# Kernel optimization log

Hardware: AMD Instinct MI355X
Metric: run time of the kernel (lower is better)

Reference implementation:

```python
import jax, jax.numpy as jnp
import numpy as np

B, S, HID = 4, 2048, 1024
NH, HD = 16, 64  # op_heads, head_size (hidden_size // total_heads)
EPS = 1e-6


def setup_inputs() -> dict:
    key = jax.random.key(0)
    k1, k2, k3, k4 = jax.random.split(key, 4)
    return {
        "hidden_states": jax.random.normal(k1, (B, S, HID), dtype=jnp.float32),
        "assoc_hc_attn": jax.random.uniform(k2, (B, S, S), dtype=jnp.float32),
        "broad_hc_attn": jax.random.uniform(k3, (B, S, S), dtype=jnp.float32),
        "Wv": jax.random.normal(k4, (HID, NH * HD), dtype=jnp.float32) * 0.02,
        "bv": jnp.zeros((NH * HD,), dtype=jnp.float32),
    }


def reference(hidden_states, assoc_hc_attn, broad_hc_attn, Wv, bv):
    # v_proj + split heads -> [B, NH, S, HD]
    value = hidden_states @ Wv + bv
    sp_value = value.reshape(B, S, NH, HD).transpose(0, 2, 1, 3)

    # broad_heads == 0, so attn_heads == assoc_hc_attn broadcast over all op_heads.
    attn = assoc_hc_attn.astype(jnp.float32)  # [B, S, S]
    causal = jnp.tril(jnp.ones((S, S), dtype=bool))
    attn = jnp.where(causal, attn, 0.0)
    # sum-normalize along keys (no softmax)
    attn = attn / (EPS + attn.sum(axis=-1, keepdims=True))

    # shared attn across heads: contract once -> [B, NH, S, HD]
    out = jnp.einsum('bqk,bhkd->bhqd', attn, sp_value)
    # merge heads -> [B, S, NH*HD]
    return out.transpose(0, 2, 1, 3).reshape(B, S, NH * HD)
```

## Files before the change

### kernel.cpp

```cpp
#include <hip/hip_runtime.h>

#define B_    4
#define S_    2048
#define HID_  1024
#define NO_   1024
#define EPS_  1e-6f
#define M1_   (B_ * S_)

typedef __attribute__((ext_vector_type(8))) short  short8;
typedef __attribute__((ext_vector_type(4))) float  f32x4;
typedef unsigned short ushort_t;

__device__ __forceinline__ unsigned short f2bf(float f) {
  union { float f; unsigned int u; } v; v.f = f;
  unsigned int r = v.u + 0x7FFFu + ((v.u >> 16) & 1u);
  return (unsigned short)(r >> 16);
}
__device__ __forceinline__ unsigned pack2(float a, float b) {
  return (unsigned)f2bf(a) | ((unsigned)f2bf(b) << 16);
}

typedef __attribute__((address_space(1))) const void GASV;
typedef __attribute__((address_space(3))) void LASV;
__device__ __forceinline__ void gld16(const void* g, void* l) {
  __builtin_amdgcn_global_load_lds((GASV*)g, (LASV*)l, 16, 0, 0);
}

__global__ __launch_bounds__(256) void k_prep(
    const float* __restrict__ Wv, ushort_t* __restrict__ WvT,
    const float* __restrict__ H,  ushort_t* __restrict__ Hb,
    const float* __restrict__ A,  ushort_t* __restrict__ Ab) {
  int id = blockIdx.x;
  if (id < 1024) {
    __shared__ float tile[32][33];
    int k0 = (id & 31) * 32;
    int n0 = (id >> 5) * 32;
    int tx = threadIdx.x & 31, ty = threadIdx.x >> 5;
    for (int i = ty; i < 32; i += 8)
      tile[i][tx] = Wv[(size_t)(k0 + i) * NO_ + n0 + tx];
    __syncthreads();
    for (int i = ty; i < 32; i += 8)
      WvT[(size_t)(n0 + i) * HID_ + k0 + tx] = f2bf(tile[tx][i]);
  } else if (id < 1024 + 8192) {
    size_t i = ((size_t)(id - 1024) * 256 + threadIdx.x) * 4;
    float4 v = *(const float4*)(H + i);
    uint2 p; p.x = pack2(v.x, v.y); p.y = pack2(v.z, v.w);
    *(uint2*)(Hb + i) = p;
  } else {
    int row  = (id - 9216) * 4 + (threadIdx.x >> 6);
    int lane = threadIdx.x & 63;
    int q = row & 2047;
    int wend = ((q >> 7) + 1) << 7;
    const float* rp = A + (size_t)row * S_;
    float4 v[8];
    float s = 0.f;
#pragma unroll
    for (int i = 0; i < 8; i++) {
      int k = i * 256 + lane * 4;
      if (k < wend) {
        float4 t = *(const float4*)(rp + k);
        t.x = (k + 0 <= q) ? t.x : 0.f;
        t.y = (k + 1 <= q) ? t.y : 0.f;
        t.z = (k + 2 <= q) ? t.z : 0.f;
        t.w = (k + 3 <= q) ? t.w : 0.f;
        v[i] = t;
        s += t.x + t.y + t.z + t.w;
      }
    }
    for (int off = 1; off < 64; off <<= 1) s += __shfl_xor(s, off, 64);
    float inv = 1.0f / (EPS_ + s);
    ushort_t* op = Ab + (size_t)row * S_;
#pragma unroll
    for (int i = 0; i < 8; i++) {
      int k = i * 256 + lane * 4;
      if (k < wend) {
        uint2 p;
        p.x = pack2(v[i].x * inv, v[i].y * inv);
        p.y = pack2(v[i].z * inv, v[i].w * inv);
        *(uint2*)(op + k) = p;
      }
    }
  }
}

__global__ __launch_bounds__(256) void k_vt(
    const ushort_t* __restrict__ WvT, const ushort_t* __restrict__ Hb,
    const float* __restrict__ bv, ushort_t* __restrict__ Vt) {
  __shared__ __align__(16) ushort_t lds_a[4 * 128 * 32];
  __shared__ __align__(16) ushort_t lds_b[4 * 128 * 32];
  int m0 = blockIdx.x * 128;
  int n0 = blockIdx.y * 128;
  int tid = threadIdx.x;
  int wave = tid >> 6, lane = tid & 63;
  int lq = lane >> 4, lm = lane & 15;
  int wr = wave >> 1, wc = wave & 1;

  int rr = lane >> 2;
  int sc = (lane & 3) ^ ((rr >> 1) & 3);
  const ushort_t* pa = WvT + (size_t)(n0 + wave * 32 + rr) * HID_ + sc * 8;
  const ushort_t* pb = Hb  + (size_t)(m0 + wave * 32 + rr) * HID_ + sc * 8;
  char* la = (char*)lds_a;
  char* lb = (char*)lds_b;
  char* la_w = la + wave * 2048;
  char* lb_w = lb + wave * 2048;
  int swz = (lm >> 1) & 3;
  int fo = (lq ^ swz) << 4;

  auto STAGE = [&](int tile) {
    char* da = la_w + (tile & 3) * 8192;
    char* db = lb_w + (tile & 3) * 8192;
    gld16(pa,             da);
    gld16(pa + 16 * HID_, da + 1024);
    gld16(pb,             db);
    gld16(pb + 16 * HID_, db + 1024);
    pa += 32; pb += 32;
  };

  f32x4 acc[4][4];
  for (int i = 0; i < 4; i++) for (int j = 0; j < 4; j++) acc[i][j] = (f32x4)0.0f;

  const int iters = HID_ / 32;
  STAGE(0); STAGE(1); STAGE(2);
  for (int it = 0; it < iters; ++it) {
    int rem = iters - 1 - it;
    if (rem >= 3) { STAGE(it + 3); asm volatile("s_waitcnt vmcnt(12)" ::: "memory"); }
    else if (rem == 2) { asm volatile("s_waitcnt vmcnt(8)"  ::: "memory"); }
    else if (rem == 1) { asm volatile("s_waitcnt vmcnt(4)"  ::: "memory"); }
    else               { asm volatile("s_waitcnt vmcnt(0)"  ::: "memory"); }
    __builtin_amdgcn_s_barrier();
    const char* ra = la + (it & 3) * 8192;
    const char* rb = lb + (it & 3) * 8192;
    short8 af[4], bfr[4];
#pragma unroll
    for (int mi = 0; mi < 4; mi++)
      af[mi] = *(const short8*)(ra + (wr * 64 + mi * 16 + lm) * 64 + fo);
#pragma unroll
    for (int ni = 0; ni < 4; ni++)
      bfr[ni] = *(const short8*)(rb + (wc * 64 + ni * 16 + lm) * 64 + fo);
#pragma unroll
    for (int mi = 0; mi < 4; mi++)
#pragma unroll
      for (int ni = 0; ni < 4; ni++)
        acc[mi][ni] = __builtin_amdgcn_mfma_f32_16x16x32_bf16(af[mi], bfr[ni], acc[mi][ni], 0, 0, 0);
    asm volatile("" ::: "memory");
    __builtin_amdgcn_s_barrier();
  }
  for (int mi = 0; mi < 4; mi++) {
    for (int r = 0; r < 4; r++) {
      int n = n0 + wr * 64 + mi * 16 + lq * 4 + r;
      float bias = bv[n];
      for (int ni = 0; ni < 4; ni++) {
        int m = m0 + wc * 64 + ni * 16 + lm;
        int b = m >> 11;
        int s = m & 2047;
        Vt[((size_t)b * NO_ + n) * S_ + s] = f2bf(acc[mi][ni][r] + bias);
      }
    }
  }
}

__global__ __launch_bounds__(256) void k_attn(
    const ushort_t* __restrict__ Ab, const ushort_t* __restrict__ Vt,
    float* __restrict__ out) {
  __shared__ __align__(16) ushort_t lds_a[4 * 128 * 32];
  __shared__ __align__(16) ushort_t lds_b[4 * 128 * 32];
  int col = blockIdx.x;
  int n0 = (col & 7) * 128;
  int b  = col >> 3;
  int tid = threadIdx.x;
  int wave = tid >> 6, lane = tid & 63;
  int lq = lane >> 4, lm = lane & 15;
  int wr = wave >> 1, wc = wave & 1;

  int rr = lane >> 2;
  int sc = (lane & 3) ^ ((rr >> 1) & 3);
  char* la = (char*)lds_a;
  char* lb = (char*)lds_b;
  char* la_w = la + wave * 2048;
  char* lb_w = lb + wave * 2048;
  int swz = (lm >> 1) & 3;
  int fo = (lq ^ swz) << 4;

  const ushort_t* gB0 = Vt + ((size_t)(b * NO_ + n0 + wave * 32 + rr)) * S_ + sc * 8;

  for (int seg = 0; seg < 2; ++seg) {
    int t  = (seg == 0) ? (int)blockIdx.y : (15 - (int)blockIdx.y);
    int q0 = t * 128;
    const int iters = 4 * t + 4;
    const ushort_t* pa = Ab + ((size_t)(b * S_ + q0 + wave * 32 + rr)) * S_ + sc * 8;
    const ushort_t* pb = gB0;

    auto STAGE = [&](int tile) {
      char* da = la_w + (tile & 3) * 8192;
      char* db = lb_w + (tile & 3) * 8192;
      gld16(pa,           da);
      gld16(pa + 16 * S_, da + 1024);
      gld16(pb,           db);
      gld16(pb + 16 * S_, db + 1024);
      pa += 32; pb += 32;
    };

    f32x4 acc[4][4];
    for (int i = 0; i < 4; i++) for (int j = 0; j < 4; j++) acc[i][j] = (f32x4)0.0f;

    STAGE(0); STAGE(1); STAGE(2);
    for (int it = 0; it < iters; ++it) {
      int rem = iters - 1 - it;
      if (rem >= 3) { STAGE(it + 3); asm volatile("s_waitcnt vmcnt(12)" ::: "memory"); }
      else if (rem == 2) { asm volatile("s_waitcnt vmcnt(8)"  ::: "memory"); }
      else if (rem == 1) { asm volatile("s_waitcnt vmcnt(4)"  ::: "memory"); }
      else               { asm volatile("s_waitcnt vmcnt(0)"  ::: "memory"); }
      __builtin_amdgcn_s_barrier();
      const char* ra = la + (it & 3) * 8192;
      const char* rb = lb + (it & 3) * 8192;
      short8 af[4], bfr[4];
#pragma unroll
      for (int mi = 0; mi < 4; mi++)
        af[mi] = *(const short8*)(ra + (wr * 64 + mi * 16 + lm) * 64 + fo);
#pragma unroll
      for (int ni = 0; ni < 4; ni++)
        bfr[ni] = *(const short8*)(rb + (wc * 64 + ni * 16 + lm) * 64 + fo);
#pragma unroll
      for (int mi = 0; mi < 4; mi++)
#pragma unroll
        for (int ni = 0; ni < 4; ni++)
          acc[mi][ni] = __builtin_amdgcn_mfma_f32_16x16x32_bf16(af[mi], bfr[ni], acc[mi][ni], 0, 0, 0);
      asm volatile("" ::: "memory");
      __builtin_amdgcn_s_barrier();
    }
    for (int mi = 0; mi < 4; mi++) {
      for (int r = 0; r < 4; r++) {
        int q = q0 + wr * 64 + mi * 16 + lq * 4 + r;
        for (int ni = 0; ni < 4; ni++) {
          int n = n0 + wc * 64 + ni * 16 + lm;
          out[((size_t)(b * S_ + q)) * NO_ + n] = acc[mi][ni][r];
        }
      }
    }
    asm volatile("s_waitcnt vmcnt(0)" ::: "memory");
  }
}

extern "C" void kernel_launch(void* const* d_in, const int* in_sizes, int n_in,
                              void* d_out, int out_size, void* d_ws, size_t ws_size,
                              hipStream_t stream) {
  const float* H  = (const float*)d_in[0];
  const float* A  = (const float*)d_in[1];
  const float* Wv = (const float*)d_in[3];
  const float* bv = (const float*)d_in[4];
  float* out = (float*)d_out;

  char* ws = (char*)d_ws;
  ushort_t* WvT = (ushort_t*)ws;
  ushort_t* Hb  = (ushort_t*)(ws + 2097152);
  ushort_t* Vt  = (ushort_t*)(ws + 2097152 + 16777216);
  ushort_t* Abf = (ushort_t*)(ws + 2097152 + 2 * 16777216);

  k_prep <<<1024 + 8192 + 2048, 256, 0, stream>>>(Wv, WvT, H, Hb, A, Abf);
  k_vt   <<<dim3(M1_ / 128, NO_ / 128), 256, 0, stream>>>(WvT, Hb, bv, Vt);
  k_attn <<<dim3(32, 8), 256, 0, stream>>>(Abf, Vt, out);
}
```

Baseline: 235.0 us.

## Use 512-thread 256x128 tiles with XCD-aware block mapping in both GEMMs

```diff
diff --git a/kernel.cpp b/kernel.cpp
--- a/kernel.cpp
+++ b/kernel.cpp
@@ -83,34 +83,36 @@
   }
 }
 
-__global__ __launch_bounds__(256) void k_vt(
+__global__ __launch_bounds__(512) void k_vt(
     const ushort_t* __restrict__ WvT, const ushort_t* __restrict__ Hb,
     const float* __restrict__ bv, ushort_t* __restrict__ Vt) {
   __shared__ __align__(16) ushort_t lds_a[4 * 128 * 32];
-  __shared__ __align__(16) ushort_t lds_b[4 * 128 * 32];
-  int m0 = blockIdx.x * 128;
-  int n0 = blockIdx.y * 128;
+  __shared__ __align__(16) ushort_t lds_b[4 * 256 * 32];
+  int id = blockIdx.x;
+  int xcd  = id & 7;
+  int mem  = id >> 3;
+  int n0   = (mem & 7) * 128;
+  int m0   = (xcd + (mem >> 3) * 8) * 256;
   int tid = threadIdx.x;
   int wave = tid >> 6, lane = tid & 63;
   int lq = lane >> 4, lm = lane & 15;
-  int wr = wave >> 1, wc = wave & 1;
+  int wm = wave >> 1, wn = wave & 1;
 
   int rr = lane >> 2;
   int sc = (lane & 3) ^ ((rr >> 1) & 3);
-  const ushort_t* pa = WvT + (size_t)(n0 + wave * 32 + rr) * HID_ + sc * 8;
+  const ushort_t* pa = WvT + (size_t)(n0 + wave * 16 + rr) * HID_ + sc * 8;
   const ushort_t* pb = Hb  + (size_t)(m0 + wave * 32 + rr) * HID_ + sc * 8;
   char* la = (char*)lds_a;
   char* lb = (char*)lds_b;
-  char* la_w = la + wave * 2048;
+  char* la_w = la + wave * 1024;
   char* lb_w = lb + wave * 2048;
   int swz = (lm >> 1) & 3;
   int fo = (lq ^ swz) << 4;
 
   auto STAGE = [&](int tile) {
     char* da = la_w + (tile & 3) * 8192;
-    char* db = lb_w + (tile & 3) * 8192;
+    char* db = lb_w + (tile & 3) * 16384;
     gld16(pa,             da);
-    gld16(pa + 16 * HID_, da + 1024);
     gld16(pb,             db);
     gld16(pb + 16 * HID_, db + 1024);
     pa += 32; pb += 32;
@@ -123,20 +125,20 @@
   STAGE(0); STAGE(1); STAGE(2);
   for (int it = 0; it < iters; ++it) {
     int rem = iters - 1 - it;
-    if (rem >= 3) { STAGE(it + 3); asm volatile("s_waitcnt vmcnt(12)" ::: "memory"); }
-    else if (rem == 2) { asm volatile("s_waitcnt vmcnt(8)"  ::: "memory"); }
-    else if (rem == 1) { asm volatile("s_waitcnt vmcnt(4)"  ::: "memory"); }
+    if (rem >= 3) { STAGE(it + 3); asm volatile("s_waitcnt vmcnt(9)" ::: "memory"); }
+    else if (rem == 2) { asm volatile("s_waitcnt vmcnt(6)"  ::: "memory"); }
+    else if (rem == 1) { asm volatile("s_waitcnt vmcnt(3)"  ::: "memory"); }
     else               { asm volatile("s_waitcnt vmcnt(0)"  ::: "memory"); }
     __builtin_amdgcn_s_barrier();
     const char* ra = la + (it & 3) * 8192;
-    const char* rb = lb + (it & 3) * 8192;
+    const char* rb = lb + (it & 3) * 16384;
     short8 af[4], bfr[4];
 #pragma unroll
     for (int mi = 0; mi < 4; mi++)
-      af[mi] = *(const short8*)(ra + (wr * 64 + mi * 16 + lm) * 64 + fo);
+      af[mi] = *(const short8*)(ra + (wn * 64 + mi * 16 + lm) * 64 + fo);
 #pragma unroll
     for (int ni = 0; ni < 4; ni++)
-      bfr[ni] = *(const short8*)(rb + (wc * 64 + ni * 16 + lm) * 64 + fo);
+      bfr[ni] = *(const short8*)(rb + (wm * 64 + ni * 16 + lm) * 64 + fo);
 #pragma unroll
     for (int mi = 0; mi < 4; mi++)
 #pragma unroll
@@ -147,10 +149,10 @@
   }
   for (int mi = 0; mi < 4; mi++) {
     for (int r = 0; r < 4; r++) {
-      int n = n0 + wr * 64 + mi * 16 + lq * 4 + r;
+      int n = n0 + wn * 64 + mi * 16 + lq * 4 + r;
       float bias = bv[n];
       for (int ni = 0; ni < 4; ni++) {
-        int m = m0 + wc * 64 + ni * 16 + lm;
+        int m = m0 + wm * 64 + ni * 16 + lm;
         int b = m >> 11;
         int s = m & 2047;
         Vt[((size_t)b * NO_ + n) * S_ + s] = f2bf(acc[mi][ni][r] + bias);
@@ -159,85 +161,81 @@
   }
 }
 
-__global__ __launch_bounds__(256) void k_attn(
+__global__ __launch_bounds__(512) void k_attn(
     const ushort_t* __restrict__ Ab, const ushort_t* __restrict__ Vt,
     float* __restrict__ out) {
-  __shared__ __align__(16) ushort_t lds_a[4 * 128 * 32];
+  __shared__ __align__(16) ushort_t lds_a[4 * 256 * 32];
   __shared__ __align__(16) ushort_t lds_b[4 * 128 * 32];
-  int col = blockIdx.x;
-  int n0 = (col & 7) * 128;
-  int b  = col >> 3;
+  int id = blockIdx.x;
+  int xcd  = id & 7;
+  int mem  = id >> 3;
+  int n0   = (mem & 7) * 128;
+  int slot = mem >> 3;
+  int b    = xcd >> 1;
+  int t    = (((xcd & 1) ? 0x1346 : 0x0257) >> (4 * slot)) & 15;
+  int q0   = t * 256;
   int tid = threadIdx.x;
   int wave = tid >> 6, lane = tid & 63;
   int lq = lane >> 4, lm = lane & 15;
-  int wr = wave >> 1, wc = wave & 1;
+  int wq = wave >> 1, wn = wave & 1;
 
   int rr = lane >> 2;
   int sc = (lane & 3) ^ ((rr >> 1) & 3);
+  const ushort_t* pa = Ab + ((size_t)(b * S_ + q0 + wave * 32 + rr)) * S_ + sc * 8;
+  const ushort_t* pb = Vt + ((size_t)(b * NO_ + n0 + wave * 16 + rr)) * S_ + sc * 8;
   char* la = (char*)lds_a;
   char* lb = (char*)lds_b;
   char* la_w = la + wave * 2048;
-  char* lb_w = lb + wave * 2048;
+  char* lb_w = lb + wave * 1024;
   int swz = (lm >> 1) & 3;
   int fo = (lq ^ swz) << 4;
 
-  const ushort_t* gB0 = Vt + ((size_t)(b * NO_ + n0 + wave * 32 + rr)) * S_ + sc * 8;
-
-  for (int seg = 0; seg < 2; ++seg) {
-    int t  = (seg == 0) ? (int)blockIdx.y : (15 - (int)blockIdx.y);
-    int q0 = t * 128;
-    const int iters = 4 * t + 4;
-    const ushort_t* pa = Ab + ((size_t)(b * S_ + q0 + wave * 32 + rr)) * S_ + sc * 8;
-    const ushort_t* pb = gB0;
-
-    auto STAGE = [&](int tile) {
-      char* da = la_w + (tile & 3) * 8192;
-      char* db = lb_w + (tile & 3) * 8192;
-      gld16(pa,           da);
-      gld16(pa + 16 * S_, da + 1024);
-      gld16(pb,           db);
-      gld16(pb + 16 * S_, db + 1024);
-      pa += 32; pb += 32;
-    };
-
-    f32x4 acc[4][4];
-    for (int i = 0; i < 4; i++) for (int j = 0; j < 4; j++) acc[i][j] = (f32x4)0.0f;
-
-    STAGE(0); STAGE(1); STAGE(2);
-    for (int it = 0; it < iters; ++it) {
-      int rem = iters - 1 - it;
-      if (rem >= 3) { STAGE(it + 3); asm volatile("s_waitcnt vmcnt(12)" ::: "memory"); }
-      else if (rem == 2) { asm volatile("s_waitcnt vmcnt(8)"  ::: "memory"); }
-      else if (rem == 1) { asm volatile("s_waitcnt vmcnt(4)"  ::: "memory"); }
-      else               { asm volatile("s_waitcnt vmcnt(0)"  ::: "memory"); }
-      __builtin_amdgcn_s_barrier();
-      const char* ra = la + (it & 3) * 8192;
-      const char* rb = lb + (it & 3) * 8192;
-      short8 af[4], bfr[4];
-#pragma unroll
-      for (int mi = 0; mi < 4; mi++)
-        af[mi] = *(const short8*)(ra + (wr * 64 + mi * 16 + lm) * 64 + fo);
+  auto STAGE = [&](int tile) {
+    char* da = la_w + (tile & 3) * 16384;
+    char* db = lb_w + (tile & 3) * 8192;
+    gld16(pa,           da);
+    gld16(pa + 16 * S_, da + 1024);
+    gld16(pb,           db);
+    pa += 32; pb += 32;
+  };
+
+  f32x4 acc[4][4];
+  for (int i = 0; i < 4; i++) for (int j = 0; j < 4; j++) acc[i][j] = (f32x4)0.0f;
+
+  const int iters = 8 * (t + 1);
+  STAGE(0); STAGE(1); STAGE(2);
+  for (int it = 0; it < iters; ++it) {
+    int rem = iters - 1 - it;
+    if (rem >= 3) { STAGE(it + 3); asm volatile("s_waitcnt vmcnt(9)" ::: "memory"); }
+    else if (rem == 2) { asm volatile("s_waitcnt vmcnt(6)"  ::: "memory"); }
+    else if (rem == 1) { asm volatile("s_waitcnt vmcnt(3)"  ::: "memory"); }
+    else               { asm volatile("s_waitcnt vmcnt(0)"  ::: "memory"); }
+    __builtin_amdgcn_s_barrier();
+    const char* ra = la + (it & 3) * 16384;
+    const char* rb = lb + (it & 3) * 8192;
+    short8 af[4], bfr[4];
+#pragma unroll
+    for (int mi = 0; mi < 4; mi++)
+      af[mi] = *(const short8*)(ra + (wq * 64 + mi * 16 + lm) * 64 + fo);
+#pragma unroll
+    for (int ni = 0; ni < 4; ni++)
+      bfr[ni] = *(const short8*)(rb + (wn * 64 + ni * 16 + lm) * 64 + fo);
+#pragma unroll
+    for (int mi = 0; mi < 4; mi++)
 #pragma unroll
       for (int ni = 0; ni < 4; ni++)
-        bfr[ni] = *(const short8*)(rb + (wc * 64 + ni * 16 + lm) * 64 + fo);
-#pragma unroll
-      for (int mi = 0; mi < 4; mi++)
-#pragma unroll
-        for (int ni = 0; ni < 4; ni++)
-          acc[mi][ni] = __builtin_amdgcn_mfma_f32_16x16x32_bf16(af[mi], bfr[ni], acc[mi][ni], 0, 0, 0);
-      asm volatile("" ::: "memory");
-      __builtin_amdgcn_s_barrier();
-    }
-    for (int mi = 0; mi < 4; mi++) {
-      for (int r = 0; r < 4; r++) {
-        int q = q0 + wr * 64 + mi * 16 + lq * 4 + r;
-        for (int ni = 0; ni < 4; ni++) {
-          int n = n0 + wc * 64 + ni * 16 + lm;
-          out[((size_t)(b * S_ + q)) * NO_ + n] = acc[mi][ni][r];
-        }
-      }
-    }
-    asm volatile("s_waitcnt vmcnt(0)" ::: "memory");
+        acc[mi][ni] = __builtin_amdgcn_mfma_f32_16x16x32_bf16(af[mi], bfr[ni], acc[mi][ni], 0, 0, 0);
+    asm volatile("" ::: "memory");
+    __builtin_amdgcn_s_barrier();
+  }
+  for (int mi = 0; mi < 4; mi++) {
+    for (int r = 0; r < 4; r++) {
+      int q = q0 + wq * 64 + mi * 16 + lq * 4 + r;
+      for (int ni = 0; ni < 4; ni++) {
+        int n = n0 + wn * 64 + ni * 16 + lm;
+        out[((size_t)(b * S_ + q)) * NO_ + n] = acc[mi][ni][r];
+      }
+    }
   }
 }
 
@@ -257,6 +255,6 @@
   ushort_t* Abf = (ushort_t*)(ws + 2097152 + 2 * 16777216);
 
   k_prep <<<1024 + 8192 + 2048, 256, 0, stream>>>(Wv, WvT, H, Hb, A, Abf);
-  k_vt   <<<dim3(M1_ / 128, NO_ / 128), 256, 0, stream>>>(WvT, Hb, bv, Vt);
-  k_attn <<<dim3(32, 8), 256, 0, stream>>>(Abf, Vt, out);
-}
+  k_vt   <<<256, 512, 0, stream>>>(WvT, Hb, bv, Vt);
+  k_attn <<<256, 512, 0, stream>>>(Abf, Vt, out);
+}
```

Result: slower. 248.3 us (+5.7%).

## Use triple-buffered LDS, XCD-aware block mapping, setprio, and unpaired attn tiles

Applied to the files above, without the earlier changes.

```diff
diff --git a/kernel.cpp b/kernel.cpp
--- a/kernel.cpp
+++ b/kernel.cpp
@@ -86,10 +86,13 @@
 __global__ __launch_bounds__(256) void k_vt(
     const ushort_t* __restrict__ WvT, const ushort_t* __restrict__ Hb,
     const float* __restrict__ bv, ushort_t* __restrict__ Vt) {
-  __shared__ __align__(16) ushort_t lds_a[4 * 128 * 32];
-  __shared__ __align__(16) ushort_t lds_b[4 * 128 * 32];
-  int m0 = blockIdx.x * 128;
-  int n0 = blockIdx.y * 128;
+  __shared__ __align__(16) ushort_t lds_a[3 * 128 * 32];
+  __shared__ __align__(16) ushort_t lds_b[3 * 128 * 32];
+  int id = blockIdx.x;
+  int xcd = id & 7;
+  int mem = id >> 3;
+  int n0  = (mem & 7) * 128;
+  int m0  = (xcd * 8 + (mem >> 3)) * 128;
   int tid = threadIdx.x;
   int wave = tid >> 6, lane = tid & 63;
   int lq = lane >> 4, lm = lane & 15;
@@ -106,9 +109,9 @@
   int swz = (lm >> 1) & 3;
   int fo = (lq ^ swz) << 4;
 
-  auto STAGE = [&](int tile) {
-    char* da = la_w + (tile & 3) * 8192;
-    char* db = lb_w + (tile & 3) * 8192;
+  auto STAGE = [&](int buf) {
+    char* da = la_w + buf * 8192;
+    char* db = lb_w + buf * 8192;
     gld16(pa,             da);
     gld16(pa + 16 * HID_, da + 1024);
     gld16(pb,             db);
@@ -120,16 +123,16 @@
   for (int i = 0; i < 4; i++) for (int j = 0; j < 4; j++) acc[i][j] = (f32x4)0.0f;
 
   const int iters = HID_ / 32;
-  STAGE(0); STAGE(1); STAGE(2);
+  STAGE(0); STAGE(1);
+  int rbuf = 0, wbuf = 2;
   for (int it = 0; it < iters; ++it) {
     int rem = iters - 1 - it;
-    if (rem >= 3) { STAGE(it + 3); asm volatile("s_waitcnt vmcnt(12)" ::: "memory"); }
-    else if (rem == 2) { asm volatile("s_waitcnt vmcnt(8)"  ::: "memory"); }
-    else if (rem == 1) { asm volatile("s_waitcnt vmcnt(4)"  ::: "memory"); }
-    else               { asm volatile("s_waitcnt vmcnt(0)"  ::: "memory"); }
-    __builtin_amdgcn_s_barrier();
-    const char* ra = la + (it & 3) * 8192;
-    const char* rb = lb + (it & 3) * 8192;
+    if (rem >= 2)      { STAGE(wbuf); asm volatile("s_waitcnt vmcnt(8)" ::: "memory"); }
+    else if (rem == 1) { asm volatile("s_waitcnt vmcnt(4)" ::: "memory"); }
+    else               { asm volatile("s_waitcnt vmcnt(0)" ::: "memory"); }
+    __builtin_amdgcn_s_barrier();
+    const char* ra = la + rbuf * 8192;
+    const char* rb = lb + rbuf * 8192;
     short8 af[4], bfr[4];
 #pragma unroll
     for (int mi = 0; mi < 4; mi++)
@@ -137,13 +140,17 @@
 #pragma unroll
     for (int ni = 0; ni < 4; ni++)
       bfr[ni] = *(const short8*)(rb + (wc * 64 + ni * 16 + lm) * 64 + fo);
+    __builtin_amdgcn_s_setprio(1);
 #pragma unroll
     for (int mi = 0; mi < 4; mi++)
 #pragma unroll
       for (int ni = 0; ni < 4; ni++)
         acc[mi][ni] = __builtin_amdgcn_mfma_f32_16x16x32_bf16(af[mi], bfr[ni], acc[mi][ni], 0, 0, 0);
+    __builtin_amdgcn_s_setprio(0);
     asm volatile("" ::: "memory");
     __builtin_amdgcn_s_barrier();
+    rbuf = (rbuf == 2) ? 0 : rbuf + 1;
+    wbuf = (wbuf == 2) ? 0 : wbuf + 1;
   }
   for (int mi = 0; mi < 4; mi++) {
     for (int r = 0; r < 4; r++) {
@@ -162,11 +169,14 @@
 __global__ __launch_bounds__(256) void k_attn(
     const ushort_t* __restrict__ Ab, const ushort_t* __restrict__ Vt,
     float* __restrict__ out) {
-  __shared__ __align__(16) ushort_t lds_a[4 * 128 * 32];
-  __shared__ __align__(16) ushort_t lds_b[4 * 128 * 32];
+  __shared__ __align__(16) ushort_t lds_a[3 * 128 * 32];
+  __shared__ __align__(16) ushort_t lds_b[3 * 128 * 32];
   int col = blockIdx.x;
   int n0 = (col & 7) * 128;
   int b  = col >> 3;
+  int y  = (int)blockIdx.y;
+  int t  = (y < 8) ? (15 - y) : (y - 8);
+  int q0 = t * 128;
   int tid = threadIdx.x;
   int wave = tid >> 6, lane = tid & 63;
   int lq = lane >> 4, lm = lane & 15;
@@ -174,6 +184,8 @@
 
   int rr = lane >> 2;
   int sc = (lane & 3) ^ ((rr >> 1) & 3);
+  const ushort_t* pa = Ab + ((size_t)(b * S_ + q0 + wave * 32 + rr)) * S_ + sc * 8;
+  const ushort_t* pb = Vt + ((size_t)(b * NO_ + n0 + wave * 32 + rr)) * S_ + sc * 8;
   char* la = (char*)lds_a;
   char* lb = (char*)lds_b;
   char* la_w = la + wave * 2048;
@@ -181,63 +193,57 @@
   int swz = (lm >> 1) & 3;
   int fo = (lq ^ swz) << 4;
 
-  const ushort_t* gB0 = Vt + ((size_t)(b * NO_ + n0 + wave * 32 + rr)) * S_ + sc * 8;
-
-  for (int seg = 0; seg < 2; ++seg) {
-    int t  = (seg == 0) ? (int)blockIdx.y : (15 - (int)blockIdx.y);
-    int q0 = t * 128;
-    const int iters = 4 * t + 4;
-    const ushort_t* pa = Ab + ((size_t)(b * S_ + q0 + wave * 32 + rr)) * S_ + sc * 8;
-    const ushort_t* pb = gB0;
-
-    auto STAGE = [&](int tile) {
-      char* da = la_w + (tile & 3) * 8192;
-      char* db = lb_w + (tile & 3) * 8192;
-      gld16(pa,           da);
-      gld16(pa + 16 * S_, da + 1024);
-      gld16(pb,           db);
-      gld16(pb + 16 * S_, db + 1024);
-      pa += 32; pb += 32;
-    };
-
-    f32x4 acc[4][4];
-    for (int i = 0; i < 4; i++) for (int j = 0; j < 4; j++) acc[i][j] = (f32x4)0.0f;
-
-    STAGE(0); STAGE(1); STAGE(2);
-    for (int it = 0; it < iters; ++it) {
-      int rem = iters - 1 - it;
-      if (rem >= 3) { STAGE(it + 3); asm volatile("s_waitcnt vmcnt(12)" ::: "memory"); }
-      else if (rem == 2) { asm volatile("s_waitcnt vmcnt(8)"  ::: "memory"); }
-      else if (rem == 1) { asm volatile("s_waitcnt vmcnt(4)"  ::: "memory"); }
-      else               { asm volatile("s_waitcnt vmcnt(0)"  ::: "memory"); }
-      __builtin_amdgcn_s_barrier();
-      const char* ra = la + (it & 3) * 8192;
-      const char* rb = lb + (it & 3) * 8192;
-      short8 af[4], bfr[4];
-#pragma unroll
-      for (int mi = 0; mi < 4; mi++)
-        af[mi] = *(const short8*)(ra + (wr * 64 + mi * 16 + lm) * 64 + fo);
+  auto STAGE = [&](int buf) {
+    char* da = la_w + buf * 8192;
+    char* db = lb_w + buf * 8192;
+    gld16(pa,           da);
+    gld16(pa + 16 * S_, da + 1024);
+    gld16(pb,           db);
+    gld16(pb + 16 * S_, db + 1024);
+    pa += 32; pb += 32;
+  };
+
+  f32x4 acc[4][4];
+  for (int i = 0; i < 4; i++) for (int j = 0; j < 4; j++) acc[i][j] = (f32x4)0.0f;
+
+  const int iters = 4 * t + 4;
+  STAGE(0); STAGE(1);
+  int rbuf = 0, wbuf = 2;
+  for (int it = 0; it < iters; ++it) {
+    int rem = iters - 1 - it;
+    if (rem >= 2)      { STAGE(wbuf); asm volatile("s_waitcnt vmcnt(8)" ::: "memory"); }
+    else if (rem == 1) { asm volatile("s_waitcnt vmcnt(4)" ::: "memory"); }
+    else               { asm volatile("s_waitcnt vmcnt(0)" ::: "memory"); }
+    __builtin_amdgcn_s_barrier();
+    const char* ra = la + rbuf * 8192;
+    const char* rb = lb + rbuf * 8192;
+    short8 af[4], bfr[4];
+#pragma unroll
+    for (int mi = 0; mi < 4; mi++)
+      af[mi] = *(const short8*)(ra + (wr * 64 + mi * 16 + lm) * 64 + fo);
+#pragma unroll
+    for (int ni = 0; ni < 4; ni++)
+      bfr[ni] = *(const short8*)(rb + (wc * 64 + ni * 16 + lm) * 64 + fo);
+    __builtin_amdgcn_s_setprio(1);
+#pragma unroll
+    for (int mi = 0; mi < 4; mi++)
 #pragma unroll
       for (int ni = 0; ni < 4; ni++)
-        bfr[ni] = *(const short8*)(rb + (wc * 64 + ni * 16 + lm) * 64 + fo);
-#pragma unroll
-      for (int mi = 0; mi < 4; mi++)
-#pragma unroll
-        for (int ni = 0; ni < 4; ni++)
-          acc[mi][ni] = __builtin_amdgcn_mfma_f32_16x16x32_bf16(af[mi], bfr[ni], acc[mi][ni], 0, 0, 0);
-      asm volatile("" ::: "memory");
-      __builtin_amdgcn_s_barrier();
-    }
-    for (int mi = 0; mi < 4; mi++) {
-      for (int r = 0; r < 4; r++) {
-        int q = q0 + wr * 64 + mi * 16 + lq * 4 + r;
-        for (int ni = 0; ni < 4; ni++) {
-          int n = n0 + wc * 64 + ni * 16 + lm;
-          out[((size_t)(b * S_ + q)) * NO_ + n] = acc[mi][ni][r];
-        }
-      }
-    }
-    asm volatile("s_waitcnt vmcnt(0)" ::: "memory");
+        acc[mi][ni] = __builtin_amdgcn_mfma_f32_16x16x32_bf16(af[mi], bfr[ni], acc[mi][ni], 0, 0, 0);
+    __builtin_amdgcn_s_setprio(0);
+    asm volatile("" ::: "memory");
+    __builtin_amdgcn_s_barrier();
+    rbuf = (rbuf == 2) ? 0 : rbuf + 1;
+    wbuf = (wbuf == 2) ? 0 : wbuf + 1;
+  }
+  for (int mi = 0; mi < 4; mi++) {
+    for (int r = 0; r < 4; r++) {
+      int q = q0 + wr * 64 + mi * 16 + lq * 4 + r;
+      for (int ni = 0; ni < 4; ni++) {
+        int n = n0 + wc * 64 + ni * 16 + lm;
+        out[((size_t)(b * S_ + q)) * NO_ + n] = acc[mi][ni][r];
+      }
+    }
   }
 }
 
@@ -257,6 +263,6 @@
   ushort_t* Abf = (ushort_t*)(ws + 2097152 + 2 * 16777216);
 
   k_prep <<<1024 + 8192 + 2048, 256, 0, stream>>>(Wv, WvT, H, Hb, A, Abf);
-  k_vt   <<<dim3(M1_ / 128, NO_ / 128), 256, 0, stream>>>(WvT, Hb, bv, Vt);
-  k_attn <<<dim3(32, 8), 256, 0, stream>>>(Abf, Vt, out);
-}
+  k_vt   <<<512, 256, 0, stream>>>(WvT, Hb, bv, Vt);
+  k_attn <<<dim3(32, 16), 256, 0, stream>>>(Abf, Vt, out);
+}
```

Measured after the change: 239.4 us. About the same (+1.9%).
